# Optimization experiments

Measured on AMD Instinct MI355X. Metric: run time of the kernel, lower is better.

## Reference

```python
import jax, jax.numpy as jnp
from jax import lax
import numpy as np

UNITS = 128
IN_DIM = 512
BATCH = 128
SEQ = 1024


def setup_inputs() -> dict:
    key = jax.random.key(0)
    k1, k2, k3 = jax.random.split(key, 3)
    x = jax.random.normal(k1, (BATCH, SEQ, IN_DIM), dtype=jnp.float32)
    # glorot-ish scaling for stability
    W = jax.random.normal(k2, (IN_DIM, 4 * UNITS), dtype=jnp.float32) * (1.0 / np.sqrt(IN_DIM))
    U = jax.random.normal(k3, (UNITS, 4 * UNITS), dtype=jnp.float32) * (1.0 / np.sqrt(UNITS))
    b = jnp.zeros((4 * UNITS,), dtype=jnp.float32)
    return {"x": x, "W": W, "U": U, "b": b}


def reference(x, W, U, b):
    # Keras LSTM with activation='tanh' AND recurrent_activation='tanh'
    # (all four gates use tanh, unlike the standard sigmoid gates).
    # Gate order in Keras kernels: i, f, g(cell candidate), o.
    B = x.shape[0]
    units = U.shape[0]
    # Precompute input projections for all timesteps: [T, B, 4*units]
    xW = jnp.einsum('bti,ij->tbj', x, W) + b

    def step(carry, xw_t):
        h, c = carry
        z = xw_t + h @ U  # [B, 4*units]
        i, f, g, o = jnp.split(z, 4, axis=-1)
        i = jnp.tanh(i)
        f = jnp.tanh(f)
        g = jnp.tanh(g)
        o = jnp.tanh(o)
        c_new = f * c + i * g
        h_new = o * jnp.tanh(c_new)
        return (h_new, c_new), None

    h0 = jnp.zeros((B, units), dtype=x.dtype)
    c0 = jnp.zeros((B, units), dtype=x.dtype)
    (h_last, _), _ = lax.scan(step, (h0, c0), xW)
    return h_last  # [B, units] (return_sequences=False)
```

## Files before the change

kernel.cpp:

```cpp
#include <hip/hip_runtime.h>
#include <hip/hip_bf16.h>


#define UNITS 128
#define IN_DIM 512
#define BATCH 128
#define SEQ 1024
#define GATES 512
#define M_ROWS (BATCH * SEQ)

typedef __attribute__((ext_vector_type(8))) short short8;
typedef __attribute__((ext_vector_type(4))) float floatx4;

__device__ __forceinline__ unsigned short f2bf(float f) {
    unsigned int x = __builtin_bit_cast(unsigned int, f);
    unsigned int r = (x + 0x7fffu + ((x >> 16) & 1u)) >> 16;
    return (unsigned short)r;
}
__device__ __forceinline__ float bf2f(unsigned short u) {
    unsigned int x = ((unsigned int)u) << 16;
    return __builtin_bit_cast(float, x);
}
__device__ __forceinline__ unsigned int pack2(float lo, float hi) {
    return (unsigned int)f2bf(lo) | ((unsigned int)f2bf(hi) << 16);
}

__device__ __forceinline__ float fast_tanh(float x) {
    float xc = fminf(12.0f, fmaxf(-12.0f, x));
    float e = __expf(2.0f * xc);
    return 1.0f - 2.0f * __builtin_amdgcn_rcpf(e + 1.0f);
}

__global__ void k_wt(const float* __restrict__ W, unsigned short* __restrict__ Wt) {
    int idx = blockIdx.x * 256 + threadIdx.x;
    int n = idx >> 9;
    int k = idx & 511;
    Wt[idx] = f2bf(W[k * 512 + n]);
}

template <bool XWF32>
__global__ void __launch_bounds__(256, 2)
k_gemm(const float* __restrict__ A, const unsigned short* __restrict__ Bt,
       void* __restrict__ Cout) {
    __shared__ __align__(16) unsigned short As[128 * 40];
    __shared__ __align__(16) unsigned short Bs[128 * 40];
    const int tid = threadIdx.x;
    const int m0 = blockIdx.y << 7;
    const int n0 = blockIdx.x << 7;
    const int l = tid & 63;
    const int w = tid >> 6;
    const int wr = (w >> 1) << 6;
    const int wc = (w & 1) << 6;
    const int lrow = l & 15;
    const int lq = l >> 4;

    floatx4 acc[4][4] = {};

    const int srow = tid >> 1;
    const int soff = (tid & 1) << 4;
    const float* ap = A + (size_t)(m0 + srow) * 512 + soff;
    const unsigned short* bp = Bt + (size_t)(n0 + srow) * 512 + soff;
    unsigned short* as = &As[srow * 40 + soff];
    unsigned short* bs = &Bs[srow * 40 + soff];

    for (int k0 = 0; k0 < 512; k0 += 32) {
        float4 a0 = *(const float4*)(ap + k0);
        float4 a1 = *(const float4*)(ap + k0 + 4);
        float4 a2 = *(const float4*)(ap + k0 + 8);
        float4 a3 = *(const float4*)(ap + k0 + 12);
        uint4 b0 = *(const uint4*)(bp + k0);
        uint4 b1 = *(const uint4*)(bp + k0 + 8);
        __syncthreads();
        uint4 pa0, pa1;
        pa0.x = pack2(a0.x, a0.y); pa0.y = pack2(a0.z, a0.w);
        pa0.z = pack2(a1.x, a1.y); pa0.w = pack2(a1.z, a1.w);
        pa1.x = pack2(a2.x, a2.y); pa1.y = pack2(a2.z, a2.w);
        pa1.z = pack2(a3.x, a3.y); pa1.w = pack2(a3.z, a3.w);
        *(uint4*)as = pa0;
        *(uint4*)(as + 8) = pa1;
        *(uint4*)bs = b0;
        *(uint4*)(bs + 8) = b1;
        __syncthreads();
        short8 af[4], bfv[4];
#pragma unroll
        for (int mi = 0; mi < 4; ++mi)
            af[mi] = *(const short8*)&As[(wr + mi * 16 + lrow) * 40 + lq * 8];
#pragma unroll
        for (int ni = 0; ni < 4; ++ni)
            bfv[ni] = *(const short8*)&Bs[(wc + ni * 16 + lrow) * 40 + lq * 8];
#pragma unroll
        for (int mi = 0; mi < 4; ++mi)
#pragma unroll
            for (int ni = 0; ni < 4; ++ni)
                acc[mi][ni] = __builtin_amdgcn_mfma_f32_16x16x32_bf16(
                    af[mi], bfv[ni], acc[mi][ni], 0, 0, 0);
    }
#pragma unroll
    for (int mi = 0; mi < 4; ++mi) {
#pragma unroll
        for (int ni = 0; ni < 4; ++ni) {
            int row = m0 + wr + mi * 16 + lq * 4;
            int col = n0 + wc + ni * 16 + lrow;
            if (XWF32) {
                float* Cf = (float*)Cout;
#pragma unroll
                for (int r = 0; r < 4; ++r)
                    Cf[(size_t)(row + r) * 512 + col] = acc[mi][ni][r];
            } else {
                unsigned short* Cb = (unsigned short*)Cout;
#pragma unroll
                for (int r = 0; r < 4; ++r)
                    Cb[(size_t)(row + r) * 512 + col] = f2bf(acc[mi][ni][r]);
            }
        }
    }
}

template <bool XWF32>
__global__ void __launch_bounds__(512, 2)
k_scan(const void* __restrict__ xwv, const float* __restrict__ U,
       const float* __restrict__ bias, float* __restrict__ out) {
    __shared__ __align__(16) float h_lds[UNITS];
    __shared__ float g_lds[GATES];
    const int j = threadIdx.x;
    const int bb = blockIdx.x;

    float u_reg[128];
#pragma unroll
    for (int k = 0; k < 128; ++k) u_reg[k] = U[k * 512 + j];
    const float bj = bias[j];
    if (j < UNITS) h_lds[j] = 0.0f;
    float c = 0.0f;
    __syncthreads();

    const float* xwf = (const float*)xwv + (size_t)bb * SEQ * 512 + j;
    const unsigned short* xwb = (const unsigned short*)xwv + (size_t)bb * SEQ * 512 + j;

    float xw_cur = XWF32 ? xwf[0] : bf2f(xwb[0]);
    for (int t = 0; t < SEQ; ++t) {
        float xw_next = 0.0f;
        if (t + 1 < SEQ)
            xw_next = XWF32 ? xwf[(size_t)(t + 1) * 512] : bf2f(xwb[(size_t)(t + 1) * 512]);

        float acc0 = 0.0f, acc1 = 0.0f;
        const float4* h4 = (const float4*)h_lds;
#pragma unroll
        for (int k4 = 0; k4 < 32; ++k4) {
            float4 hv = h4[k4];
            acc0 = fmaf(hv.x, u_reg[4 * k4 + 0], acc0);
            acc1 = fmaf(hv.y, u_reg[4 * k4 + 1], acc1);
            acc0 = fmaf(hv.z, u_reg[4 * k4 + 2], acc0);
            acc1 = fmaf(hv.w, u_reg[4 * k4 + 3], acc1);
        }
        float z = xw_cur + bj + (acc0 + acc1);
        g_lds[j] = fast_tanh(z);
        __syncthreads();
        if (j < UNITS) {
            float gi = g_lds[j];
            float gf = g_lds[128 + j];
            float gg = g_lds[256 + j];
            float go = g_lds[384 + j];
            c = fmaf(gf, c, gi * gg);
            h_lds[j] = go * fast_tanh(c);
        }
        __syncthreads();
        xw_cur = xw_next;
    }
    if (j < UNITS) out[bb * UNITS + j] = h_lds[j];
}

extern "C" void kernel_launch(void* const* d_in, const int* in_sizes, int n_in,
                              void* d_out, int out_size, void* d_ws, size_t ws_size,
                              hipStream_t stream) {
    const float* x = (const float*)d_in[0];
    const float* W = (const float*)d_in[1];
    const float* U = (const float*)d_in[2];
    const float* b = (const float*)d_in[3];
    float* out = (float*)d_out;

    char* ws = (char*)d_ws;
    const size_t WT_BYTES = (size_t)512 * 512 * 2;
    unsigned short* Wt = (unsigned short*)ws;
    void* xw = (void*)(ws + WT_BYTES);
    const size_t XW_F32_BYTES = (size_t)M_ROWS * 512 * 4;
    const bool f32path = (ws_size >= WT_BYTES + XW_F32_BYTES);

    k_wt<<<dim3(1024), dim3(256), 0, stream>>>(W, Wt);

    dim3 ggrid(4, 1024);
    if (f32path) {
        k_gemm<true><<<ggrid, dim3(256), 0, stream>>>(x, Wt, xw);
        k_scan<true><<<dim3(128), dim3(512), 0, stream>>>(xw, U, b, out);
    } else {
        k_gemm<false><<<ggrid, dim3(256), 0, stream>>>(x, Wt, xw);
        k_scan<false><<<dim3(128), dim3(512), 0, stream>>>(xw, U, b, out);
    }
}
```

Before: 1.278 ms.

## Use split-bf16 MFMA for recurrence and restructure input-projection GEMM

The scan kernel replaces the per-thread FP32 dot product over U held in registers with MFMA bf16 matrix ops. U is split into hi and lo bf16 parts, and h is split the same way, to keep near-fp32 accuracy. Each step now needs one barrier instead of two, the h buffer is double-buffered, and xW values are prefetched four steps ahead. The GEMM is reshaped so each 64-row block covers all 512 output columns, with B fragments read directly from global memory and loads software-pipelined. A new kernel transposes U. The cost is extra MFMA work for the hi/lo products, and h still carries bf16 rounding of its low part.

```diff
diff --git a/kernel.cpp b/kernel.cpp
--- a/kernel.cpp
+++ b/kernel.cpp
@@ -38,69 +38,73 @@
     Wt[idx] = f2bf(W[k * 512 + n]);
 }
 
+__global__ void k_ut(const float* __restrict__ U, float* __restrict__ Ut) {
+    int idx = blockIdx.x * 256 + threadIdx.x;
+    int col = idx >> 7;
+    int k = idx & 127;
+    Ut[idx] = U[k * 512 + col];
+}
+
 template <bool XWF32>
-__global__ void __launch_bounds__(256, 2)
-k_gemm(const float* __restrict__ A, const unsigned short* __restrict__ Bt,
-       void* __restrict__ Cout) {
-    __shared__ __align__(16) unsigned short As[128 * 40];
-    __shared__ __align__(16) unsigned short Bs[128 * 40];
+__global__ void __launch_bounds__(512, 2)
+k_gemm2(const float* __restrict__ A, const unsigned short* __restrict__ Bt,
+        void* __restrict__ Cout) {
+    __shared__ __align__(16) unsigned short As[64 * 40];
     const int tid = threadIdx.x;
-    const int m0 = blockIdx.y << 7;
-    const int n0 = blockIdx.x << 7;
+    const int m0 = blockIdx.x << 6;
     const int l = tid & 63;
     const int w = tid >> 6;
-    const int wr = (w >> 1) << 6;
-    const int wc = (w & 1) << 6;
     const int lrow = l & 15;
     const int lq = l >> 4;
 
+    const int srow = tid >> 3;
+    const int scol = (tid & 7) << 2;
+    const float* ap = A + (size_t)(m0 + srow) * 512 + scol;
+    unsigned short* as = &As[srow * 40 + scol];
+    const unsigned short* bp = Bt + (size_t)((w << 6) + lrow) * 512 + lq * 8;
+
     floatx4 acc[4][4] = {};
 
-    const int srow = tid >> 1;
-    const int soff = (tid & 1) << 4;
-    const float* ap = A + (size_t)(m0 + srow) * 512 + soff;
-    const unsigned short* bp = Bt + (size_t)(n0 + srow) * 512 + soff;
-    unsigned short* as = &As[srow * 40 + soff];
-    unsigned short* bs = &Bs[srow * 40 + soff];
+    float4 a_nx = *(const float4*)ap;
+    short8 b_nx[4];
+#pragma unroll
+    for (int ni = 0; ni < 4; ++ni)
+        b_nx[ni] = *(const short8*)(bp + ni * (16 * 512));
 
     for (int k0 = 0; k0 < 512; k0 += 32) {
-        float4 a0 = *(const float4*)(ap + k0);
-        float4 a1 = *(const float4*)(ap + k0 + 4);
-        float4 a2 = *(const float4*)(ap + k0 + 8);
-        float4 a3 = *(const float4*)(ap + k0 + 12);
-        uint4 b0 = *(const uint4*)(bp + k0);
-        uint4 b1 = *(const uint4*)(bp + k0 + 8);
+        float4 a_c = a_nx;
+        short8 b_c[4];
+#pragma unroll
+        for (int ni = 0; ni < 4; ++ni) b_c[ni] = b_nx[ni];
         __syncthreads();
-        uint4 pa0, pa1;
-        pa0.x = pack2(a0.x, a0.y); pa0.y = pack2(a0.z, a0.w);
-        pa0.z = pack2(a1.x, a1.y); pa0.w = pack2(a1.z, a1.w);
-        pa1.x = pack2(a2.x, a2.y); pa1.y = pack2(a2.z, a2.w);
-        pa1.z = pack2(a3.x, a3.y); pa1.w = pack2(a3.z, a3.w);
-        *(uint4*)as = pa0;
-        *(uint4*)(as + 8) = pa1;
-        *(uint4*)bs = b0;
-        *(uint4*)(bs + 8) = b1;
+        uint2 pa;
+        pa.x = pack2(a_c.x, a_c.y);
+        pa.y = pack2(a_c.z, a_c.w);
+        *(uint2*)as = pa;
         __syncthreads();
-        short8 af[4], bfv[4];
+        if (k0 + 32 < 512) {
+            a_nx = *(const float4*)(ap + k0 + 32);
+#pragma unroll
+            for (int ni = 0; ni < 4; ++ni)
+                b_nx[ni] = *(const short8*)(bp + ni * (16 * 512) + k0 + 32);
+        }
+        short8 af[4];
 #pragma unroll
         for (int mi = 0; mi < 4; ++mi)
-            af[mi] = *(const short8*)&As[(wr + mi * 16 + lrow) * 40 + lq * 8];
-#pragma unroll
-        for (int ni = 0; ni < 4; ++ni)
-            bfv[ni] = *(const short8*)&Bs[(wc + ni * 16 + lrow) * 40 + lq * 8];
+            af[mi] = *(const short8*)&As[(mi * 16 + lrow) * 40 + lq * 8];
 #pragma unroll
         for (int mi = 0; mi < 4; ++mi)
 #pragma unroll
             for (int ni = 0; ni < 4; ++ni)
                 acc[mi][ni] = __builtin_amdgcn_mfma_f32_16x16x32_bf16(
-                    af[mi], bfv[ni], acc[mi][ni], 0, 0, 0);
+                    af[mi], b_c[ni], acc[mi][ni], 0, 0, 0);
     }
 #pragma unroll
     for (int mi = 0; mi < 4; ++mi) {
 #pragma unroll
         for (int ni = 0; ni < 4; ++ni) {
-            int row = m0 + wr + mi * 16 + lq * 4;
-            int col = n0 + wc + ni * 16 + lrow;
+            int row = m0 + mi * 16 + lq * 4;
+            int col = (w << 6) + ni * 16 + lrow;
             if (XWF32) {
                 float* Cf = (float*)Cout;
 #pragma unroll
@@ -116,57 +120,108 @@
     }
 }
 
+#define XW_LOAD(T, g)                                                          \
+    (XWF32 ? xwf[(size_t)(T) * 512 + (g) * 128]                                \
+           : bf2f(xwb[(size_t)(T) * 512 + (g) * 128]))
+
+#define LSTM_STEP(T, S, P)                                                     \
+    {                                                                          \
+        short8 af[4];                                                          \
+        _Pragma("unroll") for (int c = 0; c < 4; ++c)                          \
+            af[c] = *(const short8*)&h2[P][n & 1][c * 32 + q * 8];             \
+        floatx4 zsum[4];                                                       \
+        _Pragma("unroll") for (int g = 0; g < 4; ++g) {                        \
+            floatx4 ah = {0.f, 0.f, 0.f, 0.f};                                 \
+            floatx4 al = {0.f, 0.f, 0.f, 0.f};                                 \
+            _Pragma("unroll") for (int c = 0; c < 4; ++c)                      \
+                ah = __builtin_amdgcn_mfma_f32_16x16x32_bf16(af[c], Bhi[g][c], \
+                                                             ah, 0, 0, 0);     \
+            _Pragma("unroll") for (int c = 0; c < 4; ++c)                      \
+                al = __builtin_amdgcn_mfma_f32_16x16x32_bf16(af[c], Blo[g][c], \
+                                                             al, 0, 0, 0);     \
+            zsum[g] = ah + al;                                                 \
+        }                                                                      \
+        float zz[4];                                                           \
+        _Pragma("unroll") for (int g = 0; g < 4; ++g)                          \
+            zz[g] = xbuf[S][g] + b4[g] + (zsum[g][0] + zsum[g][1]);            \
+        if ((T) + 4 < SEQ) {                                                   \
+            _Pragma("unroll") for (int g = 0; g < 4; ++g)                      \
+                xbuf[S][g] = XW_LOAD((T) + 4, g);                              \
+        }                                                                      \
+        float gi_ = fast_tanh(zz[0]);                                          \
+        float gf_ = fast_tanh(zz[1]);                                          \
+        float gg_ = fast_tanh(zz[2]);                                          \
+        float go_ = fast_tanh(zz[3]);                                          \
+        c_st = fmaf(gf_, c_st, gi_ * gg_);                                     \
+        h_out = go_ * fast_tanh(c_st);                                         \
+        unsigned short hh = f2bf(h_out);                                       \
+        unsigned short hl = f2bf(h_out - bf2f(hh));                            \
+        if (l < 16) {                                                          \
+            h2[(P) ^ 1][0][(w << 4) + n] = hh;                                 \
+            h2[(P) ^ 1][1][(w << 4) + n] = hl;                                 \
+        }                                                                      \
+        __syncthreads();                                                       \
+    }
+
 template <bool XWF32>
 __global__ void __launch_bounds__(512, 2)
-k_scan(const void* __restrict__ xwv, const float* __restrict__ U,
+k_scan(const void* __restrict__ xwv, const float* __restrict__ Ut,
        const float* __restrict__ bias, float* __restrict__ out) {
-    __shared__ __align__(16) float h_lds[UNITS];
-    __shared__ float g_lds[GATES];
-    const int j = threadIdx.x;
+    __shared__ __align__(16) unsigned short h2[2][2][128];
+    const int tid = threadIdx.x;
     const int bb = blockIdx.x;
-
-    float u_reg[128];
-#pragma unroll
-    for (int k = 0; k < 128; ++k) u_reg[k] = U[k * 512 + j];
-    const float bj = bias[j];
-    if (j < UNITS) h_lds[j] = 0.0f;
-    float c = 0.0f;
+    const int l = tid & 63;
+    const int w = tid >> 6;
+    const int n = l & 15;
+    const int q = l >> 4;
+
+    short8 Bhi[4][4], Blo[4][4];
+#pragma unroll
+    for (int g = 0; g < 4; ++g) {
+        const float* up = Ut + (g * 128 + (w << 4) + n) * 128 + q * 8;
+#pragma unroll
+        for (int c = 0; c < 4; ++c) {
+            float4 v0 = *(const float4*)(up + c * 32);
+            float4 v1 = *(const float4*)(up + c * 32 + 4);
+            float vv[8] = {v0.x, v0.y, v0.z, v0.w, v1.x, v1.y, v1.z, v1.w};
+            short8 hi, lo;
+#pragma unroll
+            for (int j = 0; j < 8; ++j) {
+                unsigned short hb = f2bf(vv[j]);
+                hi[j] = (short)hb;
+                lo[j] = (short)f2bf(vv[j] - bf2f(hb));
+            }
+            Bhi[g][c] = hi;
+            Blo[g][c] = lo;
+        }
+    }
+
+    if (tid < 256) ((unsigned int*)h2)[tid] = 0;
+
+    float b4[4];
+#pragma unroll
+    for (int g = 0; g < 4; ++g) b4[g] = bias[g * 128 + (w << 4) + n];
+
+    const float* xwf = (const float*)xwv + (size_t)bb * SEQ * 512 + (w << 4) + n;
+    const unsigned short* xwb =
+        (const unsigned short*)xwv + (size_t)bb * SEQ * 512 + (w << 4) + n;
+
+    float xbuf[4][4];
+#pragma unroll
+    for (int s = 0; s < 4; ++s)
+#pragma unroll
+        for (int g = 0; g < 4; ++g) xbuf[s][g] = XW_LOAD(s, g);
+
+    float c_st = 0.0f, h_out = 0.0f;
     __syncthreads();
 
-    const float* xwf = (const float*)xwv + (size_t)bb * SEQ * 512 + j;
-    const unsigned short* xwb = (const unsigned short*)xwv + (size_t)bb * SEQ * 512 + j;
-
-    float xw_cur = XWF32 ? xwf[0] : bf2f(xwb[0]);
-    for (int t = 0; t < SEQ; ++t) {
-        float xw_next = 0.0f;
-        if (t + 1 < SEQ)
-            xw_next = XWF32 ? xwf[(size_t)(t + 1) * 512] : bf2f(xwb[(size_t)(t + 1) * 512]);
-
-        float acc0 = 0.0f, acc1 = 0.0f;
-        const float4* h4 = (const float4*)h_lds;
-#pragma unroll
-        for (int k4 = 0; k4 < 32; ++k4) {
-            float4 hv = h4[k4];
-            acc0 = fmaf(hv.x, u_reg[4 * k4 + 0], acc0);
-            acc1 = fmaf(hv.y, u_reg[4 * k4 + 1], acc1);
-            acc0 = fmaf(hv.z, u_reg[4 * k4 + 2], acc0);
-            acc1 = fmaf(hv.w, u_reg[4 * k4 + 3], acc1);
-        }
-        float z = xw_cur + bj + (acc0 + acc1);
-        g_lds[j] = fast_tanh(z);
-        __syncthreads();
-        if (j < UNITS) {
-            float gi = g_lds[j];
-            float gf = g_lds[128 + j];
-            float gg = g_lds[256 + j];
-            float go = g_lds[384 + j];
-            c = fmaf(gf, c, gi * gg);
-            h_lds[j] = go * fast_tanh(c);
-        }
-        __syncthreads();
-        xw_cur = xw_next;
-    }
-    if (j < UNITS) out[bb * UNITS + j] = h_lds[j];
+    for (int t4 = 0; t4 < SEQ; t4 += 4) {
+        LSTM_STEP(t4 + 0, 0, 0)
+        LSTM_STEP(t4 + 1, 1, 1)
+        LSTM_STEP(t4 + 2, 2, 0)
+        LSTM_STEP(t4 + 3, 3, 1)
+    }
+    if (l < 16) out[bb * UNITS + (w << 4) + n] = h_out;
 }
 
 extern "C" void kernel_launch(void* const* d_in, const int* in_sizes, int n_in,
@@ -179,20 +234,23 @@
     float* out = (float*)d_out;
 
     char* ws = (char*)d_ws;
-    const size_t WT_BYTES = (size_t)512 * 512 * 2;
     unsigned short* Wt = (unsigned short*)ws;
-    void* xw = (void*)(ws + WT_BYTES);
-    const size_t XW_F32_BYTES = (size_t)M_ROWS * 512 * 4;
-    const bool f32path = (ws_size >= WT_BYTES + XW_F32_BYTES);
+    float* Ut = (float*)(ws + 524288);
+    char* rest = ws + 524288 + 262144;
+    const size_t base = 524288 + 262144;
+    const size_t XW_F32 = (size_t)M_ROWS * 512 * 4;
 
     k_wt<<<dim3(1024), dim3(256), 0, stream>>>(W, Wt);
-
-    dim3 ggrid(4, 1024);
-    if (f32path) {
-        k_gemm<true><<<ggrid, dim3(256), 0, stream>>>(x, Wt, xw);
-        k_scan<true><<<dim3(128), dim3(512), 0, stream>>>(xw, U, b, out);
+    k_ut<<<dim3(256), dim3(256), 0, stream>>>(U, Ut);
+
+    dim3 ggrid(M_ROWS / 64);
+    if (ws_size >= base + XW_F32) {
+        float* xw = (float*)rest;
+        k_gemm2<true><<<ggrid, dim3(512), 0, stream>>>(x, Wt, xw);
+        k_scan<true><<<dim3(128), dim3(512), 0, stream>>>(xw, Ut, b, out);
     } else {
-        k_gemm<false><<<ggrid, dim3(256), 0, stream>>>(x, Wt, xw);
-        k_scan<false><<<dim3(128), dim3(512), 0, stream>>>(xw, U, b, out);
-    }
-}
+        unsigned short* xw = (unsigned short*)rest;
+        k_gemm2<false><<<ggrid, dim3(512), 0, stream>>>(x, Wt, xw);
+        k_scan<false><<<dim3(128), dim3(512), 0, stream>>>(xw, Ut, b, out);
+    }
+}
```

After: 1.339 ms. +4.8%, slower.
